# Optimization experiments

Hardware: AMD Instinct MI355X
Metric: run time of the kernel (lower is better)

Reference implementation:

```python
import jax, jax.numpy as jnp
import numpy as np

EPS = 1e-5  # torch LayerNorm default

def layernorm(x, gamma, beta):
    mu = jnp.mean(x, axis=-1, keepdims=True)
    var = jnp.mean(jnp.square(x - mu), axis=-1, keepdims=True)
    return (x - mu) * jax.lax.rsqrt(var + EPS) * gamma + beta

def setup_inputs() -> dict:
    key = jax.random.key(0)
    ks = jax.random.split(key, 8)
    B, S, D = 4, 2048, 1024
    s = 1.0 / np.sqrt(D)  # torch Linear init scale
    return {
        "x": jax.random.normal(ks[0], (B, S, D), dtype=jnp.float32),
        "Wq": jax.random.uniform(ks[1], (D, D), jnp.float32, -s, s),
        "bq": jax.random.uniform(ks[2], (D,), jnp.float32, -s, s),
        "Wk": jax.random.uniform(ks[3], (D, D), jnp.float32, -s, s),
        "bk": jax.random.uniform(ks[4], (D,), jnp.float32, -s, s),
        "Wv": jax.random.uniform(ks[5], (D, D), jnp.float32, -s, s),
        "bv": jax.random.uniform(ks[6], (D,), jnp.float32, -s, s),
        "gamma": jnp.ones((D,), jnp.float32),
        "beta": jnp.zeros((D,), jnp.float32),
    }

def reference(x, Wq, bq, Wk, bk, Wv, bv, gamma, beta):
    # torch Linear: x @ W.T + b; shared LayerNorm applied to each projection
    q = layernorm(jnp.einsum('bsd,ed->bse', x, Wq) + bq, gamma, beta)
    k = layernorm(jnp.einsum('bsd,ed->bse', x, Wk) + bk, gamma, beta)
    v = layernorm(jnp.einsum('bsd,ed->bse', x, Wv) + bv, gamma, beta)
    att = jnp.einsum('bqd,bkd->bqk', q, k)  # no 1/sqrt(d) scaling in original
    att = jax.nn.softmax(att, axis=-1)
    # dropout is identity in eval mode (reference baseline)
    return jnp.einsum('bqk,bkd->bqd', att, v)
```

## Files before the change

### kernel.cpp

```cpp
#include <hip/hip_runtime.h>

typedef _Float16 f16;
typedef __attribute__((ext_vector_type(4))) _Float16 f16x4;
typedef __attribute__((ext_vector_type(8))) _Float16 f16x8;
typedef __attribute__((ext_vector_type(4))) float f32x4;

#define GLB_AS __attribute__((address_space(1)))
#define LDS_AS __attribute__((address_space(3)))

__device__ __forceinline__ void async_copy16(const void* g, void* l) {
  __builtin_amdgcn_global_load_lds((const GLB_AS void*)g, (LDS_AS void*)l, 16, 0, 0);
}

template <typename OutT>
__global__ __launch_bounds__(256) void gemm_kn(
    const f16* __restrict__ A, const f16* __restrict__ B, OutT* __restrict__ C,
    int lda, int ldb, int ldc, int K, long sA, long sB, long sC)
{
  constexpr int BM = 128, BK = 32;
  __shared__ __align__(16) f16 Ash[BM * BK];
  __shared__ __align__(16) f16 Bsh[BM * BK];

  A += (long)blockIdx.z * sA;
  B += (long)blockIdx.z * sB;
  C += (long)blockIdx.z * sC;

  const int tid  = threadIdx.x;
  const int wave = tid >> 6, lane = tid & 63;
  const int m0 = blockIdx.y * BM, n0 = blockIdx.x * BM;
  const int wm = (wave >> 1) * 64, wn = (wave & 1) * 64;

  const int srow = wave * 32 + (lane >> 2);
  const int skb  = (lane & 3) * 8;
  const f16* Ag = A + (long)(m0 + srow) * lda + skb;
  const f16* Bg = B + (long)(n0 + srow) * ldb + skb;
  f16* As0 = &Ash[(wave * 32) * BK];
  f16* As1 = &Ash[(wave * 32 + 16) * BK];
  f16* Bs0 = &Bsh[(wave * 32) * BK];
  f16* Bs1 = &Bsh[(wave * 32 + 16) * BK];

  f32x4 acc[4][4] = {};
  const int r16 = lane & 15, quad = lane >> 4;

  for (int k0 = 0; k0 < K; k0 += BK) {
    async_copy16(Ag + k0,                  As0);
    async_copy16(Ag + k0 + 16 * (long)lda, As1);
    async_copy16(Bg + k0,                  Bs0);
    async_copy16(Bg + k0 + 16 * (long)ldb, Bs1);
    __syncthreads();

    f16x8 af[4], bf[4];
#pragma unroll
    for (int i = 0; i < 4; i++) {
      af[i] = *(const f16x8*)&Ash[(wm + i * 16 + r16) * BK + quad * 8];
      bf[i] = *(const f16x8*)&Bsh[(wn + i * 16 + r16) * BK + quad * 8];
    }
#pragma unroll
    for (int i = 0; i < 4; i++)
#pragma unroll
      for (int j = 0; j < 4; j++)
        acc[i][j] = __builtin_amdgcn_mfma_f32_16x16x32_f16(af[i], bf[j], acc[i][j], 0, 0, 0);
    __syncthreads();
  }

#pragma unroll
  for (int i = 0; i < 4; i++)
#pragma unroll
    for (int j = 0; j < 4; j++)
#pragma unroll
      for (int r = 0; r < 4; r++) {
        long row = m0 + wm + i * 16 + quad * 4 + r;
        long col = n0 + wn + j * 16 + r16;
        C[row * (long)ldc + col] = (OutT)acc[i][j][r];
      }
}

__global__ __launch_bounds__(256) void cvt_f32_f16(const float* __restrict__ x,
                                                   f16* __restrict__ y, long n)
{
  long i = ((long)blockIdx.x * 256 + threadIdx.x) * 4;
  if (i >= n) return;
  const float4 v = *(const float4*)(x + i);
  f16x4 o;
  o.x = (f16)v.x; o.y = (f16)v.y; o.z = (f16)v.z; o.w = (f16)v.w;
  *(f16x4*)(y + i) = o;
}

__global__ __launch_bounds__(256) void ln_kernel(
    f16* __restrict__ P, const float* __restrict__ bq, const float* __restrict__ bk,
    const float* __restrict__ bv, const float* __restrict__ gamma,
    const float* __restrict__ beta)
{
  const int h = blockIdx.y;
  const float* bias = (h == 0) ? bq : (h == 1) ? bk : bv;
  f16* p = P + (long)h * 8388608 + (long)blockIdx.x * 1024;
  const int tid = threadIdx.x;
  const int e = tid * 4;

  f16x4 raw = *(const f16x4*)(p + e);
  float4 bb = *(const float4*)(bias + e);
  float v0 = (float)raw.x + bb.x, v1 = (float)raw.y + bb.y;
  float v2 = (float)raw.z + bb.z, v3 = (float)raw.w + bb.w;
  float s  = v0 + v1 + v2 + v3;
  float s2 = v0 * v0 + v1 * v1 + v2 * v2 + v3 * v3;

#pragma unroll
  for (int off = 32; off > 0; off >>= 1) {
    s  += __shfl_down(s, off, 64);
    s2 += __shfl_down(s2, off, 64);
  }
  __shared__ float red[10];
  const int wave = tid >> 6, lane = tid & 63;
  if (lane == 0) { red[wave] = s; red[4 + wave] = s2; }
  __syncthreads();
  if (tid == 0) {
    red[8] = red[0] + red[1] + red[2] + red[3];
    red[9] = red[4] + red[5] + red[6] + red[7];
  }
  __syncthreads();
  const float mu   = red[8] * (1.f / 1024.f);
  const float var  = red[9] * (1.f / 1024.f) - mu * mu;
  const float rstd = rsqrtf(var + 1e-5f);

  float4 gg = *(const float4*)(gamma + e);
  float4 be = *(const float4*)(beta + e);
  f16x4 o;
  o.x = (f16)((v0 - mu) * rstd * gg.x + be.x);
  o.y = (f16)((v1 - mu) * rstd * gg.y + be.y);
  o.z = (f16)((v2 - mu) * rstd * gg.z + be.z);
  o.w = (f16)((v3 - mu) * rstd * gg.w + be.w);
  *(f16x4*)(p + e) = o;
}

__global__ __launch_bounds__(256) void transpose_kernel(const f16* __restrict__ V,
                                                        f16* __restrict__ Vt)
{
  const int S = 2048, D = 1024;
  const f16* v = V + (long)blockIdx.z * ((long)S * D);
  f16* vt = Vt + (long)blockIdx.z * ((long)D * S);
  __shared__ f16 tile[64][66];
  const int d0 = blockIdx.x * 64, j0 = blockIdx.y * 64;
  const int tx = threadIdx.x & 63, ty = threadIdx.x >> 6;
#pragma unroll
  for (int r = ty; r < 64; r += 4)
    tile[r][tx] = v[(long)(j0 + r) * D + d0 + tx];
  __syncthreads();
#pragma unroll
  for (int r = ty; r < 64; r += 4)
    vt[(long)(d0 + r) * S + j0 + tx] = tile[tx][r];
}

__global__ __launch_bounds__(256) void softmax_kernel(float* __restrict__ Sc)
{
  float* srow = Sc + (long)blockIdx.x * 2048;
  const int tid = threadIdx.x;
  float4 a = ((const float4*)srow)[tid];
  float4 b = ((const float4*)srow)[256 + tid];

  float m = fmaxf(fmaxf(fmaxf(a.x, a.y), fmaxf(a.z, a.w)),
                  fmaxf(fmaxf(b.x, b.y), fmaxf(b.z, b.w)));
#pragma unroll
  for (int off = 32; off > 0; off >>= 1) m = fmaxf(m, __shfl_down(m, off, 64));
  __shared__ float red[6];
  const int wave = tid >> 6, lane = tid & 63;
  if (lane == 0) red[wave] = m;
  __syncthreads();
  if (tid == 0) red[4] = fmaxf(fmaxf(red[0], red[1]), fmaxf(red[2], red[3]));
  __syncthreads();
  const float M = red[4];

  a.x = __expf(a.x - M); a.y = __expf(a.y - M);
  a.z = __expf(a.z - M); a.w = __expf(a.w - M);
  b.x = __expf(b.x - M); b.y = __expf(b.y - M);
  b.z = __expf(b.z - M); b.w = __expf(b.w - M);
  float s = a.x + a.y + a.z + a.w + b.x + b.y + b.z + b.w;
#pragma unroll
  for (int off = 32; off > 0; off >>= 1) s += __shfl_down(s, off, 64);
  if (lane == 0) red[wave] = s;
  __syncthreads();
  if (tid == 0) red[5] = red[0] + red[1] + red[2] + red[3];
  __syncthreads();
  const float inv = 1.0f / red[5];

  f16* orow = (f16*)srow;
  f16x4 oa, ob;
  oa.x = (f16)(a.x * inv); oa.y = (f16)(a.y * inv);
  oa.z = (f16)(a.z * inv); oa.w = (f16)(a.w * inv);
  ob.x = (f16)(b.x * inv); ob.y = (f16)(b.y * inv);
  ob.z = (f16)(b.z * inv); ob.w = (f16)(b.w * inv);
  ((f16x4*)orow)[tid]       = oa;
  ((f16x4*)orow)[256 + tid] = ob;
}

extern "C" void kernel_launch(void* const* d_in, const int* in_sizes, int n_in,
                              void* d_out, int out_size, void* d_ws, size_t ws_size,
                              hipStream_t stream)
{
  const float* x     = (const float*)d_in[0];
  const float* Wq    = (const float*)d_in[1];
  const float* bq    = (const float*)d_in[2];
  const float* Wk    = (const float*)d_in[3];
  const float* bk    = (const float*)d_in[4];
  const float* Wv    = (const float*)d_in[5];
  const float* bv    = (const float*)d_in[6];
  const float* gamma = (const float*)d_in[7];
  const float* beta  = (const float*)d_in[8];
  float* out = (float*)d_out;

  char* ws = (char*)d_ws;
  f16*   P  = (f16*)(ws);
  f16*   Vt = (f16*)(ws + (48u << 20));
  float* Sc = (float*)(ws + (64u << 20));
  f16*   Xh = (f16*)(ws + (64u << 20));
  f16*   Wh = (f16*)(ws + (80u << 20));

  cvt_f32_f16<<<8192, 256, 0, stream>>>(x, Xh, 8388608L);
  cvt_f32_f16<<<1024, 256, 0, stream>>>(Wq, Wh,           1048576L);
  cvt_f32_f16<<<1024, 256, 0, stream>>>(Wk, Wh + 1048576, 1048576L);
  cvt_f32_f16<<<1024, 256, 0, stream>>>(Wv, Wh + 2097152, 1048576L);

  gemm_kn<f16><<<dim3(8, 64, 3), 256, 0, stream>>>(
      Xh, Wh, P, 1024, 1024, 1024, 1024, 0L, 1048576L, 8388608L);

  ln_kernel<<<dim3(8192, 3), 256, 0, stream>>>(P, bq, bk, bv, gamma, beta);

  transpose_kernel<<<dim3(16, 32, 4), 256, 0, stream>>>(P + 2L * 8388608, Vt);

  gemm_kn<float><<<dim3(16, 16, 4), 256, 0, stream>>>(
      P, P + 8388608, Sc, 1024, 1024, 2048, 1024, 2097152L, 2097152L, 4194304L);

  softmax_kernel<<<8192, 256, 0, stream>>>(Sc);

  gemm_kn<float><<<dim3(8, 16, 4), 256, 0, stream>>>(
      (const f16*)Sc, Vt, out, 4096, 2048, 1024, 2048, 8388608L, 2097152L, 2097152L);
}
```

Measured before the change: 353.2 us.

## Remap GEMM blocks per XCD, fold bias into epilogue, merge cast kernels

GEMM launches become 1D grids whose block index is remapped. In MODE 1, the low three bits of the block id (the XCD under round-robin dispatch) select the batch and half of the row tiles, so each XCD's L2 keeps reusing the same A and B panels. The projection GEMM now adds the per-projection bias in its fp32 epilogue before the fp16 store, and the layernorm kernel no longer reads bias. The four fp32-to-fp16 cast launches are merged into a single kernel. Together these aim to cut L2 misses and launch overhead, at the cost of extra integer index math in the GEMM prologue.

Result: faster. 333.2 us (-5.7%).

```diff
diff --git a/kernel.cpp b/kernel.cpp
--- a/kernel.cpp
+++ b/kernel.cpp
@@ -12,22 +12,41 @@
   __builtin_amdgcn_global_load_lds((const GLB_AS void*)g, (LDS_AS void*)l, 16, 0, 0);
 }
 
-template <typename OutT>
+template <typename OutT, int MODE, bool BIAS>
 __global__ __launch_bounds__(256) void gemm_kn(
     const f16* __restrict__ A, const f16* __restrict__ B, OutT* __restrict__ C,
-    int lda, int ldb, int ldc, int K, long sA, long sB, long sC)
+    int lda, int ldb, int ldc, int K, long sA, long sB, long sC,
+    int tiles_x, int tiles_y,
+    const float* __restrict__ b0, const float* __restrict__ b1,
+    const float* __restrict__ b2)
 {
   constexpr int BM = 128, BK = 32;
   __shared__ __align__(16) f16 Ash[BM * BK];
   __shared__ __align__(16) f16 Bsh[BM * BK];
 
-  A += (long)blockIdx.z * sA;
-  B += (long)blockIdx.z * sB;
-  C += (long)blockIdx.z * sC;
+  int bx, by, bz;
+  {
+    const int n = blockIdx.x;
+    if (MODE == 0) {
+      by = n % tiles_y;
+      const int r = n / tiles_y;
+      bx = r % tiles_x;
+      bz = r / tiles_x;
+    } else {
+      const int j = n & 7, i = n >> 3;
+      bz = j >> 1;
+      bx = i >> 3;
+      by = (j & 1) * 8 + (i & 7);
+    }
+  }
+
+  A += (long)bz * sA;
+  B += (long)bz * sB;
+  C += (long)bz * sC;
 
   const int tid  = threadIdx.x;
   const int wave = tid >> 6, lane = tid & 63;
-  const int m0 = blockIdx.y * BM, n0 = blockIdx.x * BM;
+  const int m0 = by * BM, n0 = bx * BM;
   const int wm = (wave >> 1) * 64, wn = (wave & 1) * 64;
 
   const int srow = wave * 32 + (lane >> 2);
@@ -63,6 +82,12 @@
     __syncthreads();
   }
 
+  float bias_j[4] = {0.f, 0.f, 0.f, 0.f};
+  if (BIAS) {
+    const float* bias = (bz == 0) ? b0 : (bz == 1) ? b1 : b2;
+#pragma unroll
+    for (int j = 0; j < 4; j++) bias_j[j] = bias[n0 + wn + j * 16 + r16];
+  }
 #pragma unroll
   for (int i = 0; i < 4; i++)
 #pragma unroll
@@ -71,36 +96,45 @@
       for (int r = 0; r < 4; r++) {
         long row = m0 + wm + i * 16 + quad * 4 + r;
         long col = n0 + wn + j * 16 + r16;
-        C[row * (long)ldc + col] = (OutT)acc[i][j][r];
+        C[row * (long)ldc + col] = (OutT)(acc[i][j][r] + bias_j[j]);
       }
 }
 
-__global__ __launch_bounds__(256) void cvt_f32_f16(const float* __restrict__ x,
-                                                   f16* __restrict__ y, long n)
-{
-  long i = ((long)blockIdx.x * 256 + threadIdx.x) * 4;
-  if (i >= n) return;
-  const float4 v = *(const float4*)(x + i);
-  f16x4 o;
-  o.x = (f16)v.x; o.y = (f16)v.y; o.z = (f16)v.z; o.w = (f16)v.w;
-  *(f16x4*)(y + i) = o;
+__global__ __launch_bounds__(256) void cast_all(
+    const float* __restrict__ x, const float* __restrict__ Wq,
+    const float* __restrict__ Wk, const float* __restrict__ Wv,
+    f16* __restrict__ Xh, f16* __restrict__ Wh)
+{
+  const long off = (long)blockIdx.x * 1024 + threadIdx.x * 4;
+  const float* src;
+  f16* dst;
+  if (off < 8388608L) {
+    src = x + off;
+    dst = Xh + off;
+  } else {
+    const long o = off - 8388608L;
+    src = (o < 1048576L) ? Wq + o
+        : (o < 2097152L) ? Wk + (o - 1048576L)
+                         : Wv + (o - 2097152L);
+    dst = Wh + o;
+  }
+  const float4 v = *(const float4*)src;
+  f16x4 h;
+  h.x = (f16)v.x; h.y = (f16)v.y; h.z = (f16)v.z; h.w = (f16)v.w;
+  *(f16x4*)dst = h;
 }
 
 __global__ __launch_bounds__(256) void ln_kernel(
-    f16* __restrict__ P, const float* __restrict__ bq, const float* __restrict__ bk,
-    const float* __restrict__ bv, const float* __restrict__ gamma,
+    f16* __restrict__ P, const float* __restrict__ gamma,
     const float* __restrict__ beta)
 {
-  const int h = blockIdx.y;
-  const float* bias = (h == 0) ? bq : (h == 1) ? bk : bv;
-  f16* p = P + (long)h * 8388608 + (long)blockIdx.x * 1024;
+  f16* p = P + (long)blockIdx.y * 8388608 + (long)blockIdx.x * 1024;
   const int tid = threadIdx.x;
   const int e = tid * 4;
 
   f16x4 raw = *(const f16x4*)(p + e);
-  float4 bb = *(const float4*)(bias + e);
-  float v0 = (float)raw.x + bb.x, v1 = (float)raw.y + bb.y;
-  float v2 = (float)raw.z + bb.z, v3 = (float)raw.w + bb.w;
+  float v0 = (float)raw.x, v1 = (float)raw.y;
+  float v2 = (float)raw.z, v3 = (float)raw.w;
   float s  = v0 + v1 + v2 + v3;
   float s2 = v0 * v0 + v1 * v1 + v2 * v2 + v3 * v3;
 
@@ -214,23 +248,23 @@
   f16*   Xh = (f16*)(ws + (64u << 20));
   f16*   Wh = (f16*)(ws + (80u << 20));
 
-  cvt_f32_f16<<<8192, 256, 0, stream>>>(x, Xh, 8388608L);
-  cvt_f32_f16<<<1024, 256, 0, stream>>>(Wq, Wh,           1048576L);
-  cvt_f32_f16<<<1024, 256, 0, stream>>>(Wk, Wh + 1048576, 1048576L);
-  cvt_f32_f16<<<1024, 256, 0, stream>>>(Wv, Wh + 2097152, 1048576L);
-
-  gemm_kn<f16><<<dim3(8, 64, 3), 256, 0, stream>>>(
-      Xh, Wh, P, 1024, 1024, 1024, 1024, 0L, 1048576L, 8388608L);
-
-  ln_kernel<<<dim3(8192, 3), 256, 0, stream>>>(P, bq, bk, bv, gamma, beta);
+  cast_all<<<11264, 256, 0, stream>>>(x, Wq, Wk, Wv, Xh, Wh);
+
+  gemm_kn<f16, 0, true><<<1536, 256, 0, stream>>>(
+      Xh, Wh, P, 1024, 1024, 1024, 1024, 0L, 1048576L, 8388608L,
+      8, 64, bq, bk, bv);
+
+  ln_kernel<<<dim3(8192, 3), 256, 0, stream>>>(P, gamma, beta);
 
   transpose_kernel<<<dim3(16, 32, 4), 256, 0, stream>>>(P + 2L * 8388608, Vt);
 
-  gemm_kn<float><<<dim3(16, 16, 4), 256, 0, stream>>>(
-      P, P + 8388608, Sc, 1024, 1024, 2048, 1024, 2097152L, 2097152L, 4194304L);
+  gemm_kn<float, 1, false><<<1024, 256, 0, stream>>>(
+      P, P + 8388608, Sc, 1024, 1024, 2048, 1024, 2097152L, 2097152L, 4194304L,
+      16, 16, nullptr, nullptr, nullptr);
 
   softmax_kernel<<<8192, 256, 0, stream>>>(Sc);
 
-  gemm_kn<float><<<dim3(8, 16, 4), 256, 0, stream>>>(
-      (const f16*)Sc, Vt, out, 4096, 2048, 1024, 2048, 8388608L, 2097152L, 2097152L);
-}
+  gemm_kn<float, 1, false><<<512, 256, 0, stream>>>(
+      (const f16*)Sc, Vt, out, 4096, 2048, 1024, 2048, 8388608L, 2097152L, 2097152L,
+      8, 16, nullptr, nullptr, nullptr);
+}
```
